# Kernel optimization log

Measured on AMD Instinct MI355X. Metric: run time of the kernel, lower is better.

## Reference

```python
import jax, jax.numpy as jnp
import numpy as np

B = 8; N_MELS = 128; T_LEN = 1024; PH = 16; PW = 16
D = 768          # embed_dim
DEPTH = 12
N = 16           # d_state
K = 4            # d_conv (mamba default)
E = 2 * D        # d_inner (expand=2)
R = 48           # dt_rank = ceil(D/16)
NC = 10
LP = (N_MELS // PH) * (T_LEN // PW)   # 512 patch tokens
MID = LP // 2                          # middle cls token position


def layer_norm(x, w, b, eps=1e-5):
    m = x.mean(-1, keepdims=True)
    v = ((x - m) ** 2).mean(-1, keepdims=True)
    return (x - m) * jax.lax.rsqrt(v + eps) * w + b


def dw_conv(x, w, b):
    # x: (B,L,E), w: (E,K) -> causal depthwise conv1d + SiLU (mamba conv branch)
    xt = jnp.transpose(x, (0, 2, 1))
    y = jax.lax.conv_general_dilated(xt, w[:, None, :], (1,), [(K - 1, 0)],
                                     feature_group_count=E,
                                     dimension_numbers=('NCH', 'OIH', 'NCH'))
    return jax.nn.silu(jnp.transpose(y + b[None, :, None], (0, 2, 1)))


def ssm(u, z, xw, dtw, dtb, A_log, Dp):
    # selective scan: u,z (B,L,E); xw (R+2N,E); dtw (E,R); A_log,Dp (E,N)/(E,)
    dbc = jnp.einsum('ble,re->blr', u, xw)
    dt, Bm, Cm = dbc[..., :R], dbc[..., R:R + N], dbc[..., R + N:]
    delta = jax.nn.softplus(jnp.einsum('blr,er->ble', dt, dtw) + dtb)
    A = -jnp.exp(A_log)  # (E,N)

    def step(h, inp):
        d_t, B_t, C_t, u_t = inp  # (B,E),(B,N),(B,N),(B,E)
        h = h * jnp.exp(d_t[:, :, None] * A) + (d_t * u_t)[:, :, None] * B_t[:, None, :]
        return h, jnp.einsum('ben,bn->be', h, C_t)

    h0 = jnp.zeros((u.shape[0], E, N), u.dtype)
    xs = (jnp.transpose(delta, (1, 0, 2)), jnp.transpose(Bm, (1, 0, 2)),
          jnp.transpose(Cm, (1, 0, 2)), jnp.transpose(u, (1, 0, 2)))
    _, ys = jax.lax.scan(step, h0, xs)
    y = jnp.transpose(ys, (1, 0, 2)) + u * Dp
    return y * jax.nn.silu(z)


def setup_inputs() -> dict:
    key = jax.random.key(0)
    kit = iter(jax.random.split(key, 64))
    def nrm(shape, s=0.02):
        return jax.random.normal(next(kit), shape, jnp.float32) * s
    inp = {}
    inp['x'] = jax.random.normal(next(kit), (B, 1, N_MELS, T_LEN), jnp.float32)
    inp['patch_w'] = nrm((D, 1, PH, PW))
    inp['patch_b'] = jnp.zeros((D,), jnp.float32)
    inp['cls_token'] = nrm((1, 1, D))
    inp['norm_w'] = jnp.ones((DEPTH, D), jnp.float32)
    inp['norm_b'] = jnp.zeros((DEPTH, D), jnp.float32)
    inp['in_proj_w'] = nrm((DEPTH, 2 * E, D))
    for s in ('f', 'b'):
        inp['conv_w_' + s] = nrm((DEPTH, E, K), 0.1)
        inp['conv_b_' + s] = jnp.zeros((DEPTH, E), jnp.float32)
        inp['x_proj_w_' + s] = nrm((DEPTH, R + 2 * N, E))
        inp['dt_proj_w_' + s] = nrm((DEPTH, E, R), 0.1)
        dt = jnp.exp(jax.random.uniform(next(kit), (DEPTH, E), jnp.float32)
                     * (np.log(0.1) - np.log(1e-3)) + np.log(1e-3))
        inp['dt_proj_b_' + s] = jnp.log(jnp.expm1(dt))  # inverse softplus init
        inp['A_log_' + s] = jnp.broadcast_to(
            jnp.log(jnp.arange(1, N + 1, dtype=jnp.float32)), (DEPTH, E, N)) + jnp.zeros((DEPTH, E, N), jnp.float32)
        inp['D_' + s] = jnp.ones((DEPTH, E), jnp.float32)
    inp['out_proj_w'] = nrm((DEPTH, D, E))
    inp['fnorm_w'] = jnp.ones((D,), jnp.float32)
    inp['fnorm_b'] = jnp.zeros((D,), jnp.float32)
    inp['head_norm_w'] = jnp.ones((D,), jnp.float32)
    inp['head_norm_b'] = jnp.zeros((D,), jnp.float32)
    inp['head_w'] = nrm((NC, D))
    inp['head_b'] = jnp.zeros((NC,), jnp.float32)
    return inp


def reference(x, patch_w, patch_b, cls_token, norm_w, norm_b, in_proj_w,
              conv_w_f, conv_b_f, conv_w_b, conv_b_b,
              x_proj_w_f, x_proj_w_b, dt_proj_w_f, dt_proj_b_f,
              dt_proj_w_b, dt_proj_b_b, A_log_f, A_log_b, D_f, D_b,
              out_proj_w, fnorm_w, fnorm_b, head_norm_w, head_norm_b,
              head_w, head_b):
    # patch embed (Conv2d, stride = patch)
    t = jax.lax.conv_general_dilated(x, patch_w, (PH, PW), 'VALID',
                                     dimension_numbers=('NCHW', 'OIHW', 'NCHW'))
    t = t + patch_b[None, :, None, None]
    b = t.shape[0]
    tok = jnp.transpose(t.reshape(b, D, -1), (0, 2, 1))  # (B, LP, D)
    cls = jnp.broadcast_to(cls_token, (b, 1, D))
    h = jnp.concatenate([tok[:, :MID], cls, tok[:, MID:]], axis=1)  # middle cls token
    for i in range(DEPTH):
        hn = layer_norm(h, norm_w[i], norm_b[i])
        xz = jnp.einsum('bld,ed->ble', hn, in_proj_w[i])
        xm, z = xz[..., :E], xz[..., E:]
        # forward direction
        xf = dw_conv(xm, conv_w_f[i], conv_b_f[i])
        yf = ssm(xf, z, x_proj_w_f[i], dt_proj_w_f[i], dt_proj_b_f[i], A_log_f[i], D_f[i])
        # backward direction (bimamba v2): scan over flipped sequence
        xr, zr = xm[:, ::-1], z[:, ::-1]
        xb = dw_conv(xr, conv_w_b[i], conv_b_b[i])
        yb = ssm(xb, zr, x_proj_w_b[i], dt_proj_w_b[i], dt_proj_b_b[i], A_log_b[i], D_b[i])[:, ::-1]
        h = h + jnp.einsum('ble,de->bld', yf + yb, out_proj_w[i])
    h = layer_norm(h, fnorm_w, fnorm_b)
    feat = h[:, MID]  # middle cls token feature
    feat = layer_norm(feat, head_norm_w, head_norm_b)
    return jnp.einsum('bd,cd->bc', feat, head_w) + head_b
```

## Files before the change

### kernel.cpp

```cpp
#include <hip/hip_runtime.h>
#include <cstddef>
#include <cstdint>

#define NB     8
#define L_SEQ  513
#define DMODEL 768
#define EDIM   1536
#define XZDIM  3072
#define NSTATE 16
#define DBCW   80
#define RDIM   48
#define ROWS   (NB*L_SEQ)
#define RE     ((size_t)ROWS*EDIM)
#define KSPLIT_DBC 8

typedef unsigned short u16;
typedef __bf16 bf16x8 __attribute__((ext_vector_type(8)));
typedef float  f32x4  __attribute__((ext_vector_type(4)));

__device__ __forceinline__ u16 f2b(float f) {
  uint32_t x = __float_as_uint(f);
  uint32_t r = x + 0x7fffu + ((x >> 16) & 1u);
  return (u16)(r >> 16);
}

__device__ __forceinline__ void glds16(const void* g, void* l) {
  __builtin_amdgcn_global_load_lds(
      (const __attribute__((address_space(1))) uint32_t*)g,
      (__attribute__((address_space(3))) uint32_t*)l, 16, 0, 0);
}

__global__ __launch_bounds__(256) void f2b_k(const float* __restrict__ in,
                                             u16* __restrict__ out, int n)
{
  int i = (blockIdx.x*256 + threadIdx.x) * 4;
  if (i >= n) return;
  float4 v = *reinterpret_cast<const float4*>(in + i);
  ushort4 o;
  o.x = f2b(v.x); o.y = f2b(v.y); o.z = f2b(v.z); o.w = f2b(v.w);
  *reinterpret_cast<ushort4*>(out + i) = o;
}

__global__ __launch_bounds__(256) void f2b2_k(const float* __restrict__ a,
                                              const float* __restrict__ b,
                                              u16* __restrict__ oa,
                                              u16* __restrict__ ob,
                                              int n1, int n2)
{
  int i = (blockIdx.x*256 + threadIdx.x) * 4;
  if (i < n1) {
    float4 v = *reinterpret_cast<const float4*>(a + i);
    ushort4 o; o.x=f2b(v.x); o.y=f2b(v.y); o.z=f2b(v.z); o.w=f2b(v.w);
    *reinterpret_cast<ushort4*>(oa + i) = o;
  } else {
    int j = i - n1;
    if (j < n2) {
      float4 v = *reinterpret_cast<const float4*>(b + j);
      ushort4 o; o.x=f2b(v.x); o.y=f2b(v.y); o.z=f2b(v.z); o.w=f2b(v.w);
      *reinterpret_cast<ushort4*>(ob + j) = o;
    }
  }
}

__global__ __launch_bounds__(256) void cvt_dtw_k(const float* __restrict__ in,
                                                 u16* __restrict__ out, int nrows)
{
  int idx = blockIdx.x*256 + threadIdx.x;
  if (idx >= nrows*16) return;
  int row = idx >> 4, c4 = (idx & 15) * 4;
  ushort4 o; o.x = o.y = o.z = o.w = 0;
  if (c4 < RDIM) {
    float4 v = *reinterpret_cast<const float4*>(in + (size_t)row*RDIM + c4);
    o.x = f2b(v.x); o.y = f2b(v.y); o.z = f2b(v.z); o.w = f2b(v.w);
  }
  *reinterpret_cast<ushort4*>(out + (size_t)row*64 + c4) = o;
}

__global__ __launch_bounds__(256) void im2col_k(const float* __restrict__ x,
                                                u16* __restrict__ P)
{
  int idx = blockIdx.x*256 + threadIdx.x;
  int col4 = (idx & 63) * 4;
  int r = idx >> 6;
  int b = r >> 9, p = r & 511;
  int ph = p >> 6, pcol = p & 63;
  int i = col4 >> 4, j = col4 & 15;
  const float* src = x + (size_t)b*131072 + (size_t)(ph*16 + i)*1024 + pcol*16 + j;
  float4 v = *reinterpret_cast<const float4*>(src);
  ushort4 o;
  o.x = f2b(v.x); o.y = f2b(v.y); o.z = f2b(v.z); o.w = f2b(v.w);
  *reinterpret_cast<ushort4*>(P + (size_t)r*256 + col4) = o;
}

__global__ __launch_bounds__(256) void insert_k(const float* __restrict__ tokf,
                                                const float* __restrict__ cls,
                                                float* __restrict__ h)
{
  int idx = blockIdx.x*256 + threadIdx.x;
  if (idx >= ROWS*192) return;
  int d4 = (idx % 192) * 4;
  int row = idx / 192;
  int b = row / L_SEQ, l = row - b*L_SEQ;
  float4 v;
  if (l == 256) v = *reinterpret_cast<const float4*>(cls + d4);
  else {
    int p = (l < 256) ? l : l - 1;
    v = *reinterpret_cast<const float4*>(tokf + ((size_t)(b*512 + p))*DMODEL + d4);
  }
  *reinterpret_cast<float4*>(h + (size_t)row*DMODEL + d4) = v;
}

__device__ __forceinline__ void wave_reduce2(float& s, float& ss) {
  #pragma unroll
  for (int o = 32; o; o >>= 1) { s += __shfl_down(s, o); ss += __shfl_down(ss, o); }
}

__global__ __launch_bounds__(256) void layernorm_k(
    const float* __restrict__ x, const float* __restrict__ w,
    const float* __restrict__ b, u16* __restrict__ y)
{
  int row = blockIdx.x;
  const float* xr = x + (size_t)row*DMODEL;
  u16*         yr = y + (size_t)row*DMODEL;
  int t = threadIdx.x;
  float v0 = xr[t], v1 = xr[t+256], v2 = xr[t+512];
  float s = v0+v1+v2, ss = v0*v0 + v1*v1 + v2*v2;
  wave_reduce2(s, ss);
  __shared__ float sm[8];
  if ((t & 63) == 0) { sm[t>>6] = s; sm[4 + (t>>6)] = ss; }
  __syncthreads();
  s  = sm[0]+sm[1]+sm[2]+sm[3];
  ss = sm[4]+sm[5]+sm[6]+sm[7];
  float mean = s * (1.f/768.f);
  float var  = ss * (1.f/768.f) - mean*mean;
  float rstd = rsqrtf(var + 1e-5f);
  yr[t]     = f2b((v0-mean)*rstd*w[t]     + b[t]);
  yr[t+256] = f2b((v1-mean)*rstd*w[t+256] + b[t+256]);
  yr[t+512] = f2b((v2-mean)*rstd*w[t+512] + b[t+512]);
}

__global__ __launch_bounds__(256) void gemm_bf16_k(
    const u16* __restrict__ A, int lda,
    const u16* __restrict__ W, int ldw,
    float* __restrict__ C, int ldc, int M, int Ncols, int K,
    const float* __restrict__ bias, int epilogue,
    int zsplit, size_t bsA, size_t bsW, size_t bsC, size_t bsBias)
{
  __shared__ __align__(16) u16 Asl[2][4096];
  __shared__ __align__(16) u16 Wsl[2][4096];
  const int tid = threadIdx.x;
  const int bm = blockIdx.y << 7, bn = blockIdx.x << 7;
  const int wv = tid >> 6, ln = tid & 63;
  const int wr = (wv >> 1) << 6, wc = (wv & 1) << 6;

  int kb = 0, ke = K;
  {
    int zb = (int)blockIdx.z;
    int dir = zb / zsplit, kslab = zb - dir*zsplit;
    A += (size_t)dir * bsA;
    W += (size_t)dir * bsW;
    C += (size_t)dir * bsC;
    if (bias) bias += (size_t)dir * bsBias;
    if (zsplit > 1) {
      int ksl = K / zsplit;
      kb = kslab * ksl; ke = kb + ksl;
      C += (size_t)kslab * (size_t)M * (size_t)ldc;
    }
  }

  const int q0 = (ln >> 4) * 8;
  const int r0 = wv*16 + (ln & 15);
  const int r1 = (wv+4)*16 + (ln & 15);

  int ar0 = bm + r0; if (ar0 >= M) ar0 = M-1;
  int ar1 = bm + r1; if (ar1 >= M) ar1 = M-1;
  int nr0 = bn + r0; if (nr0 >= Ncols) nr0 = Ncols-1;
  int nr1 = bn + r1; if (nr1 >= Ncols) nr1 = Ncols-1;
  const u16* A0 = A + (size_t)ar0*lda + q0;
  const u16* A1 = A + (size_t)ar1*lda + q0;
  const u16* W0 = W + (size_t)nr0*ldw + q0;
  const u16* W1 = W + (size_t)nr1*ldw + q0;

  auto STAGE = [&](int buf, int k0) {
    char* ab = (char*)&Asl[buf][0];
    char* wb = (char*)&Wsl[buf][0];
    glds16(A0 + k0, ab + wv*1024);
    glds16(A1 + k0, ab + 4096 + wv*1024);
    glds16(W0 + k0, wb + wv*1024);
    glds16(W1 + k0, wb + 4096 + wv*1024);
  };

  f32x4 acc[4][4];
  #pragma unroll
  for (int m = 0; m < 4; ++m)
    #pragma unroll
    for (int n = 0; n < 4; ++n) acc[m][n] = (f32x4){0.f,0.f,0.f,0.f};

  const int niter = (ke - kb) >> 5;
  STAGE(0, kb);
  for (int it = 0; it < niter; ++it) {
    const int p = it & 1;
    if (it + 1 < niter) {
      STAGE(p ^ 1, kb + (it + 1) * 32);
      asm volatile("s_waitcnt vmcnt(4)" ::: "memory");
    } else {
      asm volatile("s_waitcnt vmcnt(0)" ::: "memory");
    }
    __builtin_amdgcn_s_barrier();
    bf16x8 fa[4], fb[4];
    #pragma unroll
    for (int m = 0; m < 4; ++m)
      fa[m] = *reinterpret_cast<const bf16x8*>(&Asl[p][((wr>>4)+m)*512 + ln*8]);
    #pragma unroll
    for (int n = 0; n < 4; ++n)
      fb[n] = *reinterpret_cast<const bf16x8*>(&Wsl[p][((wc>>4)+n)*512 + ln*8]);
    #pragma unroll
    for (int m = 0; m < 4; ++m)
      #pragma unroll
      for (int n = 0; n < 4; ++n)
        acc[m][n] = __builtin_amdgcn_mfma_f32_16x16x32_bf16(fa[m], fb[n], acc[m][n], 0, 0, 0);
    __builtin_amdgcn_s_barrier();
  }

  const int crow0 = bm + wr + ((ln >> 4) << 2);
  const int ccol0 = bn + wc + (ln & 15);
  #pragma unroll
  for (int m = 0; m < 4; ++m) {
    #pragma unroll
    for (int q = 0; q < 4; ++q) {
      int row = crow0 + m*16 + q;
      if (row >= M) continue;
      float* Cr = C + (size_t)row*ldc;
      #pragma unroll
      for (int n = 0; n < 4; ++n) {
        int col = ccol0 + n*16;
        if (col >= Ncols) continue;
        float v = acc[m][n][q];
        if (epilogue == 1) v += Cr[col];
        else if (epilogue == 2) {
          v += bias[col];
          v = fmaxf(v, 0.f) + log1pf(__expf(-fabsf(v)));
        } else if (epilogue == 3) v += bias[col];
        Cr[col] = v;
      }
    }
  }
}

__global__ void reduce_split2_k(const float* __restrict__ part,
                                float* __restrict__ dbc2, u16* __restrict__ dt48,
                                int nsplit)
{
  int i = blockIdx.x * 256 + threadIdx.x;
  if (i >= 2*ROWS*DBCW) return;
  int dir = i / (ROWS*DBCW);
  int j   = i - dir*(ROWS*DBCW);
  const float* p = part + (size_t)dir*nsplit*(ROWS*DBCW);
  float s = 0.f;
  for (int z = 0; z < nsplit; ++z) s += p[(size_t)z*(ROWS*DBCW) + j];
  dbc2[i] = s;
  int row = j / DBCW, col = j - row*DBCW;
  if (col < RDIM)    dt48[(size_t)dir*ROWS*64 + (size_t)row*64 + col] = f2b(s);
  else if (col < 64) dt48[(size_t)dir*ROWS*64 + (size_t)row*64 + col] = 0;
}

__global__ __launch_bounds__(256) void reduce4_addh_k(const float* __restrict__ part,
                                                      float* __restrict__ h)
{
  size_t i = ((size_t)blockIdx.x*256 + threadIdx.x) * 4;
  if (i >= (size_t)ROWS*DMODEL) return;
  const size_t S = (size_t)ROWS*DMODEL;
  float4 s0 = *reinterpret_cast<const float4*>(part + i);
  float4 s1 = *reinterpret_cast<const float4*>(part + S + i);
  float4 s2 = *reinterpret_cast<const float4*>(part + 2*S + i);
  float4 s3 = *reinterpret_cast<const float4*>(part + 3*S + i);
  float4 hv = *reinterpret_cast<const float4*>(h + i);
  hv.x += (s0.x + s1.x) + (s2.x + s3.x);
  hv.y += (s0.y + s1.y) + (s2.y + s3.y);
  hv.z += (s0.z + s1.z) + (s2.z + s3.z);
  hv.w += (s0.w + s1.w) + (s2.w + s3.w);
  *reinterpret_cast<float4*>(h + i) = hv;
}

__global__ __launch_bounds__(256) void dwconv_silu_k(
    const float* __restrict__ xz,
    const float* __restrict__ w_f, const float* __restrict__ w_b,
    const float* __restrict__ b_f, const float* __restrict__ b_b,
    u16* __restrict__ outb2)
{
  const int dir = blockIdx.y;
  const float* w    = dir ? w_b : w_f;
  const float* bias = dir ? b_b : b_f;
  u16* outb = outb2 + (size_t)dir*RE;
  int idx = blockIdx.x * 256 + threadIdx.x;
  int r = idx / (EDIM/4);
  int e4 = (idx - r*(EDIM/4)) * 4;
  int b = r / L_SEQ, t = r - b*L_SEQ;
  float4 acc = *reinterpret_cast<const float4*>(&bias[e4]);
  float4 wq0 = *reinterpret_cast<const float4*>(&w[(size_t)(e4+0)*4]);
  float4 wq1 = *reinterpret_cast<const float4*>(&w[(size_t)(e4+1)*4]);
  float4 wq2 = *reinterpret_cast<const float4*>(&w[(size_t)(e4+2)*4]);
  float4 wq3 = *reinterpret_cast<const float4*>(&w[(size_t)(e4+3)*4]);
  #pragma unroll
  for (int k = 0; k < 4; ++k) {
    int tt = t - 3 + k;
    if (tt >= 0) {
      int phys = dir ? (L_SEQ-1 - tt) : tt;
      float4 xv = *reinterpret_cast<const float4*>(
          &xz[((size_t)b*L_SEQ + phys)*XZDIM + e4]);
      float w0 = (k==0)?wq0.x:(k==1)?wq0.y:(k==2)?wq0.z:wq0.w;
      float w1 = (k==0)?wq1.x:(k==1)?wq1.y:(k==2)?wq1.z:wq1.w;
      float w2 = (k==0)?wq2.x:(k==1)?wq2.y:(k==2)?wq2.z:wq2.w;
      float w3 = (k==0)?wq3.x:(k==1)?wq3.y:(k==2)?wq3.z:wq3.w;
      acc.x = fmaf(xv.x, w0, acc.x);
      acc.y = fmaf(xv.y, w1, acc.y);
      acc.z = fmaf(xv.z, w2, acc.z);
      acc.w = fmaf(xv.w, w3, acc.w);
    }
  }
  float4 sv;
  sv.x = acc.x / (1.f + __expf(-acc.x));
  sv.y = acc.y / (1.f + __expf(-acc.y));
  sv.z = acc.z / (1.f + __expf(-acc.z));
  sv.w = acc.w / (1.f + __expf(-acc.w));
  ushort4 ob;
  ob.x = f2b(sv.x); ob.y = f2b(sv.y); ob.z = f2b(sv.z); ob.w = f2b(sv.w);
  *reinterpret_cast<ushort4*>(&outb[(size_t)r*EDIM + e4]) = ob;
}

__device__ __forceinline__ float dpp_reduce16(float v) {
  v += __int_as_float(__builtin_amdgcn_update_dpp(0, __float_as_int(v), 0x111, 0xf, 0xf, true));
  v += __int_as_float(__builtin_amdgcn_update_dpp(0, __float_as_int(v), 0x112, 0xf, 0xf, true));
  v += __int_as_float(__builtin_amdgcn_update_dpp(0, __float_as_int(v), 0x114, 0xf, 0xf, true));
  v += __int_as_float(__builtin_amdgcn_update_dpp(0, __float_as_int(v), 0x118, 0xf, 0xf, true));
  return v;
}

#define TC 32
#define NCH ((L_SEQ + TC - 1) / TC)

__global__ __launch_bounds__(256) void ssm_scan_k(
    const float* __restrict__ delta2, const u16* __restrict__ ub2,
    const float* __restrict__ dbc2,
    const float* __restrict__ Alf, const float* __restrict__ Alb,
    const float* __restrict__ Dpf, const float* __restrict__ Dpb,
    const float* __restrict__ xz,  u16* __restrict__ yhalf)
{
  __shared__ __align__(16) float du[2][TC][16][2];
  __shared__ __align__(16) float Bs[2][16][TC+4];
  __shared__ __align__(16) float Cs[2][16][TC+4];
  __shared__ __align__(16) float yb[TC][16];

  const int dir = blockIdx.z;
  const float* delta = delta2 + (size_t)dir*RE;
  const u16*   ub    = ub2    + (size_t)dir*RE;
  const float* dbc   = dbc2   + (size_t)dir*ROWS*DBCW;
  const float* A_log = dir ? Alb : Alf;
  const float* Dp    = dir ? Dpb : Dpf;
  u16* yh = yhalf + (size_t)dir*RE;

  const int tid = threadIdx.x;
  const int g = tid >> 4, n = tid & 15;
  const int b = blockIdx.y;
  const int e0 = blockIdx.x * 16;
  const int e = e0 + g;
  const size_t rb = (size_t)b * L_SEQ;

  const float a  = -__expf(A_log[(size_t)e*NSTATE + n]);
  const float dp = Dp[e];

  const int ss_ = tid >> 3;
  const int c2  = (tid & 7) * 2;
  const int j4  = (tid & 7) * 4;

  float2 dv = make_float2(0,0);
  uint32_t uv = 0;
  float4 bcv = make_float4(0,0,0,0);

  auto LOAD = [&](int c) {
    int Tn = min(TC, L_SEQ - c*TC);
    if (ss_ < Tn) {
      size_t r = rb + c*TC + ss_;
      dv  = *reinterpret_cast<const float2*>(&delta[r*EDIM + e0 + c2]);
      uv  = *reinterpret_cast<const uint32_t*>(&ub[r*EDIM + e0 + c2]);
      bcv = *reinterpret_cast<const float4*>(&dbc[r*DBCW + RDIM + j4]);
    }
  };
  auto STORE = [&](int p, int c) {
    int Tn = min(TC, L_SEQ - c*TC);
    if (ss_ < Tn) {
      float2 w0 = make_float2(dv.x, __uint_as_float((uv & 0xffffu) << 16));
      float2 w1 = make_float2(dv.y, __uint_as_float(uv & 0xffff0000u));
      *reinterpret_cast<float2*>(&du[p][ss_][c2][0])   = w0;
      *reinterpret_cast<float2*>(&du[p][ss_][c2+1][0]) = w1;
      if (j4 < 16) {
        Bs[p][j4  ][ss_] = bcv.x; Bs[p][j4+1][ss_] = bcv.y;
        Bs[p][j4+2][ss_] = bcv.z; Bs[p][j4+3][ss_] = bcv.w;
      } else {
        Cs[p][j4-16][ss_] = bcv.x; Cs[p][j4-15][ss_] = bcv.y;
        Cs[p][j4-14][ss_] = bcv.z; Cs[p][j4-13][ss_] = bcv.w;
      }
    }
  };

  float hst = 0.f;
  LOAD(0);
  STORE(0, 0);
  __syncthreads();

  int p = 0;
  for (int c = 0; c < NCH; ++c) {
    const int t0 = c * TC;
    const int T  = min(TC, L_SEQ - t0);
    if (c + 1 < NCH) LOAD(c + 1);

    int s = 0;
    for (; s + 3 < T; s += 4) {
      float4 Bv = *reinterpret_cast<const float4*>(&Bs[p][n][s]);
      float4 Cv = *reinterpret_cast<const float4*>(&Cs[p][n][s]);
      #pragma unroll
      for (int i = 0; i < 4; ++i) {
        float Bt = (i==0)?Bv.x:(i==1)?Bv.y:(i==2)?Bv.z:Bv.w;
        float Ct = (i==0)?Cv.x:(i==1)?Cv.y:(i==2)?Cv.z:Cv.w;
        float2 duv = *reinterpret_cast<const float2*>(&du[p][s+i][g][0]);
        float d  = duv.x;
        float uu = duv.y;
        hst = fmaf(hst, __expf(d*a), d*uu*Bt);
        float yp = dpp_reduce16(hst * Ct);
        if (n == 15) yb[s+i][g] = yp + uu*dp;
      }
    }
    for (; s < T; ++s) {
      float Bt = Bs[p][n][s], Ct = Cs[p][n][s];
      float2 duv = *reinterpret_cast<const float2*>(&du[p][s][g][0]);
      float d  = duv.x;
      float uu = duv.y;
      hst = fmaf(hst, __expf(d*a), d*uu*Bt);
      float yp = dpp_reduce16(hst * Ct);
      if (n == 15) yb[s][g] = yp + uu*dp;
    }
    __syncthreads();

    if (ss_ < T) {
      int t = t0 + ss_;
      int phys = dir ? (L_SEQ-1 - t) : t;
      size_t pr = rb + phys;
      float2 yv = *reinterpret_cast<const float2*>(&yb[ss_][c2]);
      float2 zv = *reinterpret_cast<const float2*>(&xz[pr*XZDIM + EDIM + e0 + c2]);
      ushort2 o;
      o.x = f2b(yv.x * (zv.x / (1.f + __expf(-zv.x))));
      o.y = f2b(yv.y * (zv.y / (1.f + __expf(-zv.y))));
      *reinterpret_cast<ushort2*>(&yh[pr*EDIM + e0 + c2]) = o;
    }
    if (c + 1 < NCH) STORE(p ^ 1, c + 1);
    __syncthreads();
    p ^= 1;
  }
}

__global__ __launch_bounds__(256) void add_ybf_k(const u16* __restrict__ yhalf,
                                                 u16* __restrict__ ybf)
{
  size_t i = ((size_t)blockIdx.x*256 + threadIdx.x) * 8;
  uint4 a = *reinterpret_cast<const uint4*>(yhalf + i);
  uint4 b = *reinterpret_cast<const uint4*>(yhalf + RE + i);
  uint32_t av[4] = {a.x, a.y, a.z, a.w};
  uint32_t bv[4] = {b.x, b.y, b.z, b.w};
  uint32_t ov[4];
  #pragma unroll
  for (int q = 0; q < 4; ++q) {
    float lo = __uint_as_float((av[q] & 0xffffu) << 16) +
               __uint_as_float((bv[q] & 0xffffu) << 16);
    float hi = __uint_as_float(av[q] & 0xffff0000u) +
               __uint_as_float(bv[q] & 0xffff0000u);
    ov[q] = (uint32_t)f2b(lo) | ((uint32_t)f2b(hi) << 16);
  }
  uint4 o = {ov[0], ov[1], ov[2], ov[3]};
  *reinterpret_cast<uint4*>(ybf + i) = o;
}

__global__ __launch_bounds__(256) void head_k(
    const float* __restrict__ h,
    const float* __restrict__ fnw, const float* __restrict__ fnb,
    const float* __restrict__ hnw, const float* __restrict__ hnb,
    const float* __restrict__ hw,  const float* __restrict__ hb,
    float* __restrict__ out)
{
  int b = blockIdx.x, t = threadIdx.x;
  const float* xr = h + ((size_t)b*L_SEQ + 256)*DMODEL;
  __shared__ float feat[DMODEL];
  __shared__ float sm[8];
  float v0 = xr[t], v1 = xr[t+256], v2 = xr[t+512];
  float s = v0+v1+v2, ss = v0*v0+v1*v1+v2*v2;
  wave_reduce2(s, ss);
  if ((t & 63) == 0) { sm[t>>6] = s; sm[4+(t>>6)] = ss; }
  __syncthreads();
  s = sm[0]+sm[1]+sm[2]+sm[3]; ss = sm[4]+sm[5]+sm[6]+sm[7];
  float mean = s*(1.f/768.f), var = ss*(1.f/768.f) - mean*mean;
  float rstd = rsqrtf(var + 1e-5f);
  float f0 = (v0-mean)*rstd*fnw[t]     + fnb[t];
  float f1 = (v1-mean)*rstd*fnw[t+256] + fnb[t+256];
  float f2 = (v2-mean)*rstd*fnw[t+512] + fnb[t+512];
  s = f0+f1+f2; ss = f0*f0+f1*f1+f2*f2;
  wave_reduce2(s, ss);
  __syncthreads();
  if ((t & 63) == 0) { sm[t>>6] = s; sm[4+(t>>6)] = ss; }
  __syncthreads();
  s = sm[0]+sm[1]+sm[2]+sm[3]; ss = sm[4]+sm[5]+sm[6]+sm[7];
  mean = s*(1.f/768.f); var = ss*(1.f/768.f) - mean*mean;
  rstd = rsqrtf(var + 1e-5f);
  feat[t]     = (f0-mean)*rstd*hnw[t]     + hnb[t];
  feat[t+256] = (f1-mean)*rstd*hnw[t+256] + hnb[t+256];
  feat[t+512] = (f2-mean)*rstd*hnw[t+512] + hnb[t+512];
  __syncthreads();
  for (int c = 0; c < 10; ++c) {
    float d = 0.f;
    for (int i = t; i < DMODEL; i += 256) d = fmaf(feat[i], hw[(size_t)c*DMODEL + i], d);
    #pragma unroll
    for (int o = 32; o; o >>= 1) d += __shfl_down(d, o);
    __syncthreads();
    if ((t & 63) == 0) sm[t>>6] = d;
    __syncthreads();
    if (t == 0) out[b*10 + c] = sm[0]+sm[1]+sm[2]+sm[3] + hb[c];
  }
}

extern "C" void kernel_launch(void* const* d_in, const int* in_sizes, int n_in,
                              void* d_out, int out_size, void* d_ws, size_t ws_size,
                              hipStream_t stream)
{
  (void)in_sizes; (void)n_in; (void)out_size; (void)ws_size;
  const float* x           = (const float*)d_in[0];
  const float* patch_w     = (const float*)d_in[1];
  const float* patch_b     = (const float*)d_in[2];
  const float* cls_tok     = (const float*)d_in[3];
  const float* norm_w      = (const float*)d_in[4];
  const float* norm_b      = (const float*)d_in[5];
  const float* in_proj_w   = (const float*)d_in[6];
  const float* conv_w_f    = (const float*)d_in[7];
  const float* conv_b_f    = (const float*)d_in[8];
  const float* x_proj_w_f  = (const float*)d_in[9];
  const float* dt_proj_w_f = (const float*)d_in[10];
  const float* dt_proj_b_f = (const float*)d_in[11];
  const float* A_log_f     = (const float*)d_in[12];
  const float* D_f         = (const float*)d_in[13];
  const float* conv_w_b    = (const float*)d_in[14];
  const float* conv_b_b    = (const float*)d_in[15];
  const float* x_proj_w_b  = (const float*)d_in[16];
  const float* dt_proj_w_b = (const float*)d_in[17];
  const float* dt_proj_b_b = (const float*)d_in[18];
  const float* A_log_b     = (const float*)d_in[19];
  const float* D_b         = (const float*)d_in[20];
  const float* out_proj_w  = (const float*)d_in[21];
  const float* fnorm_w     = (const float*)d_in[22];
  const float* fnorm_b     = (const float*)d_in[23];
  const float* head_norm_w = (const float*)d_in[24];
  const float* head_norm_b = (const float*)d_in[25];
  const float* head_w      = (const float*)d_in[26];
  const float* head_b      = (const float*)d_in[27];
  float* out = (float*)d_out;

  float* ws = (float*)d_ws;
  float* h      = ws;        ws += (size_t)ROWS*DMODEL;
  u16*   hn     = (u16*)ws;  ws += RE/2;
  u16*   ybf    = hn;
  float* xz     = ws;        ws += (size_t)ROWS*XZDIM;
  u16*   ubufb2 = (u16*)ws;  ws += RE;
  float* dbc2   = ws;        ws += (size_t)2*ROWS*DBCW;
  u16*   dt48b2 = (u16*)ws;  ws += (size_t)2*ROWS*64/2;
  float* delta2 = ws;        ws += 2*RE;
  u16*   yhalf  = (u16*)ws;  ws += RE;
  u16*   wbf_a  = (u16*)ws;  ws += (size_t)XZDIM*DMODEL/2;
  u16*   wbf_b  = (u16*)ws;  ws += (size_t)DMODEL*EDIM/2;
  u16*   pwbf   = (u16*)ws;  ws += (size_t)DMODEL*256/2;
  u16*   xwbf   = (u16*)ws;  ws += (size_t)2*12*DBCW*EDIM/2;
  u16*   dtwbf  = (u16*)ws;  ws += (size_t)2*12*EDIM*64/2;
  float* dtb2   = ws;        ws += (size_t)2*12*EDIM;
  float* dbcp   = delta2;
  float* opart  = delta2;
  u16*   Pim    = ubufb2;
  float* tokf   = delta2;

  f2b_k<<<(DMODEL*256)/1024, 256, 0, stream>>>(patch_w, pwbf, DMODEL*256);
  f2b_k<<<(12*DBCW*EDIM)/1024, 256, 0, stream>>>(x_proj_w_f, xwbf, 12*DBCW*EDIM);
  f2b_k<<<(12*DBCW*EDIM)/1024, 256, 0, stream>>>(x_proj_w_b, xwbf + (size_t)12*DBCW*EDIM, 12*DBCW*EDIM);
  cvt_dtw_k<<<(12*EDIM*16)/256, 256, 0, stream>>>(dt_proj_w_f, dtwbf, 12*EDIM);
  cvt_dtw_k<<<(12*EDIM*16)/256, 256, 0, stream>>>(dt_proj_w_b, dtwbf + (size_t)12*EDIM*64, 12*EDIM);
  hipMemcpyAsync(dtb2,           dt_proj_b_f, (size_t)12*EDIM*4, hipMemcpyDeviceToDevice, stream);
  hipMemcpyAsync(dtb2 + 12*EDIM, dt_proj_b_b, (size_t)12*EDIM*4, hipMemcpyDeviceToDevice, stream);

  im2col_k<<<(4096*64)/256, 256, 0, stream>>>(x, Pim);
  {
    dim3 g(DMODEL/128, 4096/128);
    gemm_bf16_k<<<g, 256, 0, stream>>>(Pim, 256, pwbf, 256, tokf, DMODEL,
                                       4096, DMODEL, 256, patch_b, 3,
                                       1, 0, 0, 0, 0);
  }
  insert_k<<<(ROWS*192 + 255)/256, 256, 0, stream>>>(tokf, cls_tok, h);

  const int MT = (ROWS + 127)/128;

  for (int i = 0; i < 12; ++i) {
    f2b2_k<<<(XZDIM*DMODEL + DMODEL*EDIM)/1024, 256, 0, stream>>>(
        in_proj_w + (size_t)i*XZDIM*DMODEL, out_proj_w + (size_t)i*DMODEL*EDIM,
        wbf_a, wbf_b, XZDIM*DMODEL, DMODEL*EDIM);
    layernorm_k<<<ROWS, 256, 0, stream>>>(h, norm_w + (size_t)i*DMODEL,
                                          norm_b + (size_t)i*DMODEL, hn);
    {
      dim3 g(XZDIM/128, MT);
      gemm_bf16_k<<<g, 256, 0, stream>>>(hn, DMODEL, wbf_a, DMODEL,
                                         xz, XZDIM, ROWS, XZDIM, DMODEL, nullptr, 0,
                                         1, 0, 0, 0, 0);
    }
    {
      dim3 g((ROWS*EDIM/4)/256, 2);
      dwconv_silu_k<<<g, 256, 0, stream>>>(xz,
          conv_w_f + (size_t)i*EDIM*4, conv_w_b + (size_t)i*EDIM*4,
          conv_b_f + (size_t)i*EDIM,   conv_b_b + (size_t)i*EDIM, ubufb2);
    }
    {
      dim3 g(1, MT, 2*KSPLIT_DBC);
      gemm_bf16_k<<<g, 256, 0, stream>>>(ubufb2, EDIM,
          xwbf + (size_t)i*DBCW*EDIM, EDIM,
          dbcp, DBCW, ROWS, DBCW, EDIM, nullptr, 0,
          KSPLIT_DBC, RE, (size_t)12*DBCW*EDIM, (size_t)KSPLIT_DBC*ROWS*DBCW, 0);
      reduce_split2_k<<<(2*ROWS*DBCW + 255)/256, 256, 0, stream>>>(
          dbcp, dbc2, dt48b2, KSPLIT_DBC);
    }
    {
      dim3 g(EDIM/128, MT, 2);
      gemm_bf16_k<<<g, 256, 0, stream>>>(dt48b2, 64,
          dtwbf + (size_t)i*EDIM*64, 64,
          delta2, EDIM, ROWS, EDIM, 64, dtb2 + (size_t)i*EDIM, 2,
          1, (size_t)ROWS*64, (size_t)12*EDIM*64, RE, (size_t)12*EDIM);
    }
    {
      dim3 g(EDIM/16, NB, 2);
      ssm_scan_k<<<g, 256, 0, stream>>>(delta2, ubufb2, dbc2,
          A_log_f + (size_t)i*EDIM*NSTATE, A_log_b + (size_t)i*EDIM*NSTATE,
          D_f + (size_t)i*EDIM, D_b + (size_t)i*EDIM, xz, yhalf);
    }
    add_ybf_k<<<(int)(RE/8/256), 256, 0, stream>>>(yhalf, ybf);
    {
      dim3 g(DMODEL/128, MT, 4);
      gemm_bf16_k<<<g, 256, 0, stream>>>(ybf, EDIM, wbf_b, EDIM,
                                         opart, DMODEL, ROWS, DMODEL, EDIM, nullptr, 0,
                                         4, 0, 0, 0, 0);
      reduce4_addh_k<<<(int)(((size_t)ROWS*DMODEL/4 + 255)/256), 256, 0, stream>>>(opart, h);
    }
  }

  head_k<<<NB, 256, 0, stream>>>(h, fnorm_w, fnorm_b, head_norm_w, head_norm_b,
                                 head_w, head_b, out);
}
```

Before: 4.438 ms.

## Fuse direction sum into out_proj split-K and fuse residual add with next LayerNorm

Result: slower. 4.604 ms (+3.7%).

```diff
diff --git a/kernel.cpp b/kernel.cpp
--- a/kernel.cpp
+++ b/kernel.cpp
@@ -264,22 +264,40 @@
   else if (col < 64) dt48[(size_t)dir*ROWS*64 + (size_t)row*64 + col] = 0;
 }
 
-__global__ __launch_bounds__(256) void reduce4_addh_k(const float* __restrict__ part,
-                                                      float* __restrict__ h)
-{
-  size_t i = ((size_t)blockIdx.x*256 + threadIdx.x) * 4;
-  if (i >= (size_t)ROWS*DMODEL) return;
+__global__ __launch_bounds__(256) void reduce4_ln_k(
+    const float* __restrict__ part, float* __restrict__ h,
+    const float* __restrict__ w, const float* __restrict__ b,
+    u16* __restrict__ y)
+{
+  int row = blockIdx.x;
+  int t = threadIdx.x;
   const size_t S = (size_t)ROWS*DMODEL;
-  float4 s0 = *reinterpret_cast<const float4*>(part + i);
-  float4 s1 = *reinterpret_cast<const float4*>(part + S + i);
-  float4 s2 = *reinterpret_cast<const float4*>(part + 2*S + i);
-  float4 s3 = *reinterpret_cast<const float4*>(part + 3*S + i);
-  float4 hv = *reinterpret_cast<const float4*>(h + i);
-  hv.x += (s0.x + s1.x) + (s2.x + s3.x);
-  hv.y += (s0.y + s1.y) + (s2.y + s3.y);
-  hv.z += (s0.z + s1.z) + (s2.z + s3.z);
-  hv.w += (s0.w + s1.w) + (s2.w + s3.w);
-  *reinterpret_cast<float4*>(h + i) = hv;
+  const size_t base = (size_t)row*DMODEL;
+  float v[3];
+  #pragma unroll
+  for (int j = 0; j < 3; ++j) {
+    size_t idx = base + t + j*256;
+    float s = (part[idx] + part[S+idx]) + (part[2*S+idx] + part[3*S+idx]);
+    s += h[idx];
+    h[idx] = s;
+    v[j] = s;
+  }
+  if (!w) return;
+  float s = v[0]+v[1]+v[2], ss = v[0]*v[0]+v[1]*v[1]+v[2]*v[2];
+  wave_reduce2(s, ss);
+  __shared__ float sm[8];
+  if ((t & 63) == 0) { sm[t>>6] = s; sm[4+(t>>6)] = ss; }
+  __syncthreads();
+  s = sm[0]+sm[1]+sm[2]+sm[3]; ss = sm[4]+sm[5]+sm[6]+sm[7];
+  float mean = s*(1.f/768.f);
+  float var  = ss*(1.f/768.f) - mean*mean;
+  float rstd = rsqrtf(var + 1e-5f);
+  u16* yr = y + base;
+  #pragma unroll
+  for (int j = 0; j < 3; ++j) {
+    int col = t + j*256;
+    yr[col] = f2b((v[j]-mean)*rstd*w[col] + b[col]);
+  }
 }
 
 __global__ __launch_bounds__(256) void dwconv_silu_k(
@@ -456,27 +474,6 @@
     __syncthreads();
     p ^= 1;
   }
-}
-
-__global__ __launch_bounds__(256) void add_ybf_k(const u16* __restrict__ yhalf,
-                                                 u16* __restrict__ ybf)
-{
-  size_t i = ((size_t)blockIdx.x*256 + threadIdx.x) * 8;
-  uint4 a = *reinterpret_cast<const uint4*>(yhalf + i);
-  uint4 b = *reinterpret_cast<const uint4*>(yhalf + RE + i);
-  uint32_t av[4] = {a.x, a.y, a.z, a.w};
-  uint32_t bv[4] = {b.x, b.y, b.z, b.w};
-  uint32_t ov[4];
-  #pragma unroll
-  for (int q = 0; q < 4; ++q) {
-    float lo = __uint_as_float((av[q] & 0xffffu) << 16) +
-               __uint_as_float((bv[q] & 0xffffu) << 16);
-    float hi = __uint_as_float(av[q] & 0xffff0000u) +
-               __uint_as_float(bv[q] & 0xffff0000u);
-    ov[q] = (uint32_t)f2b(lo) | ((uint32_t)f2b(hi) << 16);
-  }
-  uint4 o = {ov[0], ov[1], ov[2], ov[3]};
-  *reinterpret_cast<uint4*>(ybf + i) = o;
 }
 
 __global__ __launch_bounds__(256) void head_k(
@@ -563,7 +560,6 @@
   float* ws = (float*)d_ws;
   float* h      = ws;        ws += (size_t)ROWS*DMODEL;
   u16*   hn     = (u16*)ws;  ws += RE/2;
-  u16*   ybf    = hn;
   float* xz     = ws;        ws += (size_t)ROWS*XZDIM;
   u16*   ubufb2 = (u16*)ws;  ws += RE;
   float* dbc2   = ws;        ws += (size_t)2*ROWS*DBCW;
@@ -599,13 +595,14 @@
   insert_k<<<(ROWS*192 + 255)/256, 256, 0, stream>>>(tokf, cls_tok, h);
 
   const int MT = (ROWS + 127)/128;
+  const size_t S = (size_t)ROWS*DMODEL;
+
+  layernorm_k<<<ROWS, 256, 0, stream>>>(h, norm_w, norm_b, hn);
 
   for (int i = 0; i < 12; ++i) {
     f2b2_k<<<(XZDIM*DMODEL + DMODEL*EDIM)/1024, 256, 0, stream>>>(
         in_proj_w + (size_t)i*XZDIM*DMODEL, out_proj_w + (size_t)i*DMODEL*EDIM,
         wbf_a, wbf_b, XZDIM*DMODEL, DMODEL*EDIM);
-    layernorm_k<<<ROWS, 256, 0, stream>>>(h, norm_w + (size_t)i*DMODEL,
-                                          norm_b + (size_t)i*DMODEL, hn);
     {
       dim3 g(XZDIM/128, MT);
       gemm_bf16_k<<<g, 256, 0, stream>>>(hn, DMODEL, wbf_a, DMODEL,
@@ -640,13 +637,16 @@
           A_log_f + (size_t)i*EDIM*NSTATE, A_log_b + (size_t)i*EDIM*NSTATE,
           D_f + (size_t)i*EDIM, D_b + (size_t)i*EDIM, xz, yhalf);
     }
-    add_ybf_k<<<(int)(RE/8/256), 256, 0, stream>>>(yhalf, ybf);
     {
       dim3 g(DMODEL/128, MT, 4);
-      gemm_bf16_k<<<g, 256, 0, stream>>>(ybf, EDIM, wbf_b, EDIM,
+      gemm_bf16_k<<<g, 256, 0, stream>>>(yhalf, EDIM, wbf_b, EDIM,
                                          opart, DMODEL, ROWS, DMODEL, EDIM, nullptr, 0,
-                                         4, 0, 0, 0, 0);
-      reduce4_addh_k<<<(int)(((size_t)ROWS*DMODEL/4 + 255)/256), 256, 0, stream>>>(opart, h);
+                                         2, RE, 0, 2*S, 0);
+    }
+    {
+      const float* lw = (i < 11) ? (norm_w + (size_t)(i+1)*DMODEL) : nullptr;
+      const float* lb = (i < 11) ? (norm_b + (size_t)(i+1)*DMODEL) : nullptr;
+      reduce4_ln_k<<<ROWS, 256, 0, stream>>>(opart, h, lw, lb, hn);
     }
   }
 
```
